# Kernel tuning notes

Measured on AMD Instinct MI355X. Metric: run time of the kernel, lower is better.

## Reference

```python
import jax, jax.numpy as jnp
import numpy as np

N, WH, C = 8, 16384, 256
R = 4
DK = 256

def setup_inputs() -> dict:
    key = jax.random.key(0)
    ks = jax.random.split(key, 11)
    s = lambda fan_in: 1.0 / np.sqrt(fan_in)
    return {
        "x":    jax.random.normal(ks[0], (N, WH, C), dtype=jnp.float32),
        # SequenceReducer linear: in=C*R, out=C (stored as [in, out])
        "w_sr": jax.random.uniform(ks[1], (C * R, C), jnp.float32, -s(C * R), s(C * R)),
        "b_sr": jax.random.uniform(ks[2], (C,), jnp.float32, -s(C * R), s(C * R)),
        # q/k/v projections: in=C, out=DK
        "w_q":  jax.random.uniform(ks[3], (C, DK), jnp.float32, -s(C), s(C)),
        "b_q":  jax.random.uniform(ks[4], (DK,), jnp.float32, -s(C), s(C)),
        "w_k":  jax.random.uniform(ks[5], (C, DK), jnp.float32, -s(C), s(C)),
        "b_k":  jax.random.uniform(ks[6], (DK,), jnp.float32, -s(C), s(C)),
        "w_v":  jax.random.uniform(ks[7], (C, DK), jnp.float32, -s(C), s(C)),
        "b_v":  jax.random.uniform(ks[8], (DK,), jnp.float32, -s(C), s(C)),
        # out projection: in=DK, out=C*R
        "w_o":  jax.random.uniform(ks[9], (DK, C * R), jnp.float32, -s(DK), s(DK)),
        "b_o":  jax.random.uniform(ks[10], (C * R,), jnp.float32, -s(DK), s(DK)),
    }

def reference(x, w_sr, b_sr, w_q, b_q, w_k, b_k, w_v, b_v, w_o, b_o):
    n, wh, c = x.shape
    L = wh // R  # reduced sequence length
    # SequenceReducer: fold R adjacent tokens into channel dim, then linear back to C
    xr = x.reshape(n, L, c * R) @ w_sr + b_sr              # [N, L, C]
    q = xr @ w_q + b_q                                     # [N, L, DK]
    k = xr @ w_k + b_k
    v = xr @ w_v + b_v
    scale = jnp.asarray(DK ** 0.5, x.dtype)
    logits = jnp.einsum('nqd,nkd->nqk', q, k) / scale      # [N, L, L]
    attn = jax.nn.softmax(logits, axis=-1)
    o = jnp.einsum('nqk,nkd->nqd', attn, v)                # [N, L, DK]
    out = (o @ w_o + b_o).reshape(n, wh, c)                # [N, WH, C]
    return out
```

## Files before the change

### kernel.cpp

```cpp
#include <hip/hip_runtime.h>

#define DEVI __device__ __forceinline__

typedef float  f32x4  __attribute__((ext_vector_type(4)));
typedef float  f32x16 __attribute__((ext_vector_type(16)));
typedef short  s16x8  __attribute__((ext_vector_type(8)));
typedef unsigned u32x4 __attribute__((ext_vector_type(4)));

DEVI void gload16(const void* g, void* l) {
  __builtin_amdgcn_global_load_lds(
      (const __attribute__((address_space(1))) void*)g,
      (__attribute__((address_space(3))) void*)l, 16, 0, 0);
}

DEVI ushort f2b(float f) {
  unsigned u = __builtin_bit_cast(unsigned, f);
  unsigned r = (u + 0x7fffu + ((u >> 16) & 1u)) >> 16;
  return (ushort)r;
}
DEVI unsigned cvtpk(float lo, float hi) {
  unsigned r;
  asm("v_cvt_pk_bf16_f32 %0, %1, %2" : "=v"(r) : "v"(lo), "v"(hi));
  return r;
}
DEVI float b2f(short s) {
  return __builtin_bit_cast(float, (unsigned)((ushort)s) << 16);
}
DEVI float max3(float a, float b, float c) { return fmaxf(fmaxf(a, b), c); }

DEVI f32x4 mfma16(s16x8 a, s16x8 b, f32x4 c) {
  return __builtin_amdgcn_mfma_f32_16x16x32_bf16(a, b, c, 0, 0, 0);
}
DEVI f32x16 mfma32(s16x8 a, s16x8 b, f32x16 c) {
  return __builtin_amdgcn_mfma_f32_32x32x16_bf16(a, b, c, 0, 0, 0);
}

DEVI int kperm(int r) {
  return (r & 0x13) | ((r & 4) << 1) | ((r & 8) >> 1);
}

__global__ __launch_bounds__(256) void k_compose(
    const float* __restrict__ w_sr, const float* __restrict__ b_sr,
    const float* __restrict__ w_q, const float* __restrict__ b_q,
    const float* __restrict__ w_k, const float* __restrict__ b_k,
    const float* __restrict__ w_v, const float* __restrict__ b_v,
    const float* __restrict__ w_o,
    ushort* __restrict__ wqkvT, ushort* __restrict__ woT, float* __restrict__ bqkv)
{
  const int b = blockIdx.x, t = threadIdx.x;
  if (b < 256) {
    const int i0 = b * 4;
    float acc[4][3] = {};
    for (int c = 0; c < 256; ++c) {
      float wq = w_q[c * 256 + t], wk = w_k[c * 256 + t], wv = w_v[c * 256 + t];
#pragma unroll
      for (int r = 0; r < 4; ++r) {
        float a = w_sr[(i0 + r) * 256 + c];
        acc[r][0] += a * wq; acc[r][1] += a * wk; acc[r][2] += a * wv;
      }
    }
#pragma unroll
    for (int r = 0; r < 4; ++r) {
      wqkvT[(size_t)(t)       * 1024 + i0 + r] = f2b(acc[r][0]);
      wqkvT[(size_t)(256 + t) * 1024 + i0 + r] = f2b(acc[r][1]);
      wqkvT[(size_t)(512 + t) * 1024 + i0 + r] = f2b(acc[r][2]);
    }
  } else if (b == 256) {
    float a0 = b_q[t], a1 = b_k[t], a2 = b_v[t];
    for (int c = 0; c < 256; ++c) {
      float bs = b_sr[c];
      a0 += bs * w_q[c * 256 + t];
      a1 += bs * w_k[c * 256 + t];
      a2 += bs * w_v[c * 256 + t];
    }
    bqkv[t] = a0; bqkv[256 + t] = a1; bqkv[512 + t] = a2;
  } else {
    const int kk = b - 257;
#pragma unroll
    for (int n = t; n < 1024; n += 256)
      woT[(size_t)n * 256 + kk] = f2b(w_o[(size_t)kk * 1024 + n]);
  }
}

__global__ __launch_bounds__(256, 2) void k_gemm_qkv(
    const float* __restrict__ X, const ushort* __restrict__ WT,
    const float* __restrict__ bias,
    ushort* __restrict__ Qo, ushort* __restrict__ Ko, ushort* __restrict__ VTo)
{
  __shared__ float  As[128 * 32];
  __shared__ ushort Bs[256 * 32];
  const int tid = threadIdx.x;
  const int l = tid & 63, w = tid >> 6;
  const int wr = w >> 1, wc = w & 1;
  const int g = l >> 4, lr = l & 15;
  const int bx = blockIdx.x;
  const int xs = (bx & 7) * 32 + (bx >> 3);
  const int tM = xs * 128, tN = blockIdx.y * 256;
  f32x4 acc[4][8] = {};

  for (int kt = 0; kt < 32; ++kt) {
    const int k0 = kt * 32;
#pragma unroll
    for (int j = 0; j < 4; ++j) {
      int chunk = j * 256 + tid;
      int row = chunk >> 3, kc = chunk & 7;
      gload16(X + (size_t)(tM + row) * 1024 + k0 + ((kc ^ (row & 7)) << 2),
              (char*)As + (j * 256 + w * 64) * 16);
    }
#pragma unroll
    for (int j = 0; j < 4; ++j) {
      int chunk = j * 256 + tid;
      int row = chunk >> 2, kc = chunk & 3;
      gload16(WT + (size_t)(tN + row) * 1024 + k0 + ((kc ^ (row & 3)) << 3),
              (char*)Bs + (j * 256 + w * 64) * 16);
    }
    __syncthreads();
    s16x8 bfr[8];
#pragma unroll
    for (int ni = 0; ni < 8; ++ni) {
      int col = wc * 128 + ni * 16 + lr;
      bfr[ni] = *(const s16x8*)&Bs[col * 32 + ((g ^ (col & 3)) << 3)];
    }
#pragma unroll
    for (int mi = 0; mi < 4; ++mi) {
      int row = wr * 64 + mi * 16 + lr;
      int c1 = (2 * g) ^ (row & 7);
      int c2 = (2 * g + 1) ^ (row & 7);
      f32x4 a0 = *(const f32x4*)&As[row * 32 + c1 * 4];
      f32x4 a1 = *(const f32x4*)&As[row * 32 + c2 * 4];
      s16x8 af = __builtin_bit_cast(s16x8,
          (u32x4){cvtpk(a0[0], a0[1]), cvtpk(a0[2], a0[3]),
                  cvtpk(a1[0], a1[1]), cvtpk(a1[2], a1[3])});
#pragma unroll
      for (int ni = 0; ni < 8; ++ni)
        acc[mi][ni] = mfma16(af, bfr[ni], acc[mi][ni]);
    }
    __syncthreads();
  }
#pragma unroll
  for (int ni = 0; ni < 8; ++ni) {
    const int col = tN + wc * 128 + ni * 16 + lr;
    const float bv = bias[col];
#pragma unroll
    for (int mi = 0; mi < 4; ++mi) {
      const int r0 = tM + wr * 64 + mi * 16 + g * 4;
      f32x4 c = acc[mi][ni];
      if (col < 512) {
        ushort* dst = (col < 256) ? Qo : Ko;
        const int cc = col & 255;
#pragma unroll
        for (int j = 0; j < 4; ++j)
          dst[(size_t)(r0 + j) * 256 + cc] = f2b(c[j] + bv);
      } else {
        const int d = col - 512;
        const int n = r0 >> 12, lrr = r0 & 4095;
        ushort4 pv;
        pv.x = f2b(c[0] + bv); pv.y = f2b(c[1] + bv);
        pv.z = f2b(c[2] + bv); pv.w = f2b(c[3] + bv);
        *(ushort4*)&VTo[(size_t)n * 256 * 4096 + (size_t)d * 4096 + lrr] = pv;
      }
    }
  }
}

#define KSC 0.0901687369f

template<int NSPLIT>
__global__ __launch_bounds__(256, 2) void k_flash(
    const ushort* __restrict__ Qg, const ushort* __restrict__ Kg,
    const ushort* __restrict__ VTg, ushort* __restrict__ Po, float* __restrict__ MLo)
{
  __shared__ ushort Ks[2][8192];
  __shared__ ushort Vs[2][8192];
  const int tid = threadIdx.x;
  const int l = tid & 63, w = tid >> 6;
  const int by = blockIdx.x & 7;
  const int rest = blockIdx.x >> 3;
  const int split = (NSPLIT == 2) ? (rest & 1) : 0;
  const int qt = (NSPLIT == 2) ? (rest >> 1) : rest;
  const int NT = (NSPLIT == 2) ? 64 : 128;
  const int kv0 = split * 2048;
  const int q0 = qt * 128 + w * 32;
  const int cl = l & 31, h = l >> 5;
  const size_t qrow = (size_t)by * 4096 + q0 + cl;

  s16x8 qf[16];
#pragma unroll
  for (int s = 0; s < 16; ++s)
    qf[s] = *(const s16x8*)&Qg[qrow * 256 + s * 16 + h * 8];

  f32x16 ot[8] = {};
  float m_run = -1e30f, l_run = 0.0f;

  const ushort* kb0 = Kg + ((size_t)by * 4096 + kv0) * 256;
  const ushort* vb0 = VTg + (size_t)by * 256 * 4096 + kv0;

  auto stage = [&](int t, int buf) {
    const ushort* kb = kb0 + t * 32 * 256;
#pragma unroll
    for (int j = 0; j < 4; ++j) {
      int chunk = j * 256 + tid;
      gload16(kb + kperm(chunk & 31) * 256 + (chunk >> 5) * 8,
              &Ks[buf][(j * 256 + w * 64) * 8]);
    }
    const ushort* vb = vb0 + t * 32;
#pragma unroll
    for (int j = 0; j < 4; ++j) {
      int chunk = j * 256 + tid;
      gload16(vb + (size_t)(chunk & 255) * 4096 + (chunk >> 8) * 8,
              &Vs[buf][(j * 256 + w * 64) * 8]);
    }
  };

  stage(0, 0);
  __syncthreads();

  for (int t = 0; t < NT; ++t) {
    const int buf = t & 1;
    if (t + 1 < NT) stage(t + 1, buf ^ 1);
    const ushort* KT = Ks[buf];

    f32x16 sa = {};
    __builtin_amdgcn_s_setprio(1);
#pragma unroll
    for (int s = 0; s < 16; ++s) {
      s16x8 a = *(const s16x8*)&KT[(2 * s + h) * 256 + cl * 8];
      sa = mfma32(a, qf[s], sa);
    }
    __builtin_amdgcn_s_setprio(0);

    float t0 = max3(sa[0], sa[1], sa[2]);
    float t1 = max3(sa[3], sa[4], sa[5]);
    float t2 = max3(sa[6], sa[7], sa[8]);
    float t3 = max3(sa[9], sa[10], sa[11]);
    float t4 = max3(sa[12], sa[13], sa[14]);
    float pmax = fmaxf(max3(t0, t1, t2), max3(t3, t4, sa[15]));
    pmax = fmaxf(pmax, __shfl_xor(pmax, 32));
    if (!__all(pmax <= m_run + 120.0f)) {
      float m_new = fmaxf(m_run, pmax);
      float corr = exp2f((m_run - m_new) * KSC);
      l_run *= corr;
#pragma unroll
      for (int mf = 0; mf < 8; ++mf)
#pragma unroll
        for (int i = 0; i < 16; ++i) ot[mf][i] *= corr;
      m_run = m_new;
    }
    const float mK = m_run * KSC;
    unsigned pk[4][2];
    float lp = 0.0f;
#pragma unroll
    for (int gq = 0; gq < 4; ++gq) {
      float p0 = exp2f(__builtin_fmaf(sa[4 * gq + 0], KSC, -mK));
      float p1 = exp2f(__builtin_fmaf(sa[4 * gq + 1], KSC, -mK));
      float p2 = exp2f(__builtin_fmaf(sa[4 * gq + 2], KSC, -mK));
      float p3 = exp2f(__builtin_fmaf(sa[4 * gq + 3], KSC, -mK));
      lp += (p0 + p1) + (p2 + p3);
      pk[gq][0] = cvtpk(p0, p1);
      pk[gq][1] = cvtpk(p2, p3);
    }
    l_run += lp;

    const ushort* VT2 = Vs[buf];
#pragma unroll
    for (int ks = 0; ks < 2; ++ks) {
      const s16x8 pf = __builtin_bit_cast(s16x8,
          (u32x4){pk[2 * ks][0], pk[2 * ks][1], pk[2 * ks + 1][0], pk[2 * ks + 1][1]});
      __builtin_amdgcn_s_setprio(1);
#pragma unroll
      for (int mf = 0; mf < 8; ++mf) {
        s16x8 va = *(const s16x8*)&VT2[(2 * ks + h) * 2048 + (mf * 32 + cl) * 8];
        ot[mf] = mfma32(va, pf, ot[mf]);
      }
      __builtin_amdgcn_s_setprio(0);
    }
    __syncthreads();
  }

  const float l_tot = l_run + __shfl_xor(l_run, 32);
  const float rl = 1.0f / l_tot;
  const size_t orow = (size_t)split * 32768 + qrow;
#pragma unroll
  for (int mf = 0; mf < 8; ++mf)
#pragma unroll
    for (int c = 0; c < 4; ++c) {
      const int d0 = mf * 32 + 8 * c + 4 * h;
      uint2 pv;
      pv.x = cvtpk(ot[mf][4 * c + 0] * rl, ot[mf][4 * c + 1] * rl);
      pv.y = cvtpk(ot[mf][4 * c + 2] * rl, ot[mf][4 * c + 3] * rl);
      *(uint2*)&Po[orow * 256 + d0] = pv;
    }
  if (NSPLIT == 2 && h == 0) {
    float2 ml; ml.x = m_run; ml.y = l_tot;
    *(float2*)&MLo[orow * 2] = ml;
  }
}

__global__ __launch_bounds__(256) void k_combine(
    const ushort* __restrict__ P, const float* __restrict__ ML,
    ushort* __restrict__ Og)
{
  const int idx = blockIdx.x * 256 + threadIdx.x;
  const int r = idx >> 5, dc = (idx & 31) * 8;
  const float m0 = ML[(size_t)r * 2],             l0 = ML[(size_t)r * 2 + 1];
  const float m1 = ML[(size_t)(32768 + r) * 2],   l1 = ML[(size_t)(32768 + r) * 2 + 1];
  const float m  = fmaxf(m0, m1);
  const float a0 = l0 * exp2f((m0 - m) * KSC);
  const float a1 = l1 * exp2f((m1 - m) * KSC);
  const float inv = 1.0f / (a0 + a1);
  const float w0 = a0 * inv, w1 = a1 * inv;
  s16x8 x0 = *(const s16x8*)&P[(size_t)r * 256 + dc];
  s16x8 x1 = *(const s16x8*)&P[(size_t)(32768 + r) * 256 + dc];
  union { ushort u[8]; s16x8 v; } o;
#pragma unroll
  for (int j = 0; j < 8; ++j)
    o.u[j] = f2b(w0 * b2f(x0[j]) + w1 * b2f(x1[j]));
  *(s16x8*)&Og[(size_t)r * 256 + dc] = o.v;
}

__global__ __launch_bounds__(256, 2) void k_gemm_out(
    const ushort* __restrict__ Oi, const ushort* __restrict__ WT,
    const float* __restrict__ bias, float* __restrict__ OUT)
{
  __shared__ ushort As[128 * 32];
  __shared__ ushort Bs[256 * 32];
  const int tid = threadIdx.x;
  const int l = tid & 63, w = tid >> 6;
  const int wr = w >> 1, wc = w & 1;
  const int g = l >> 4, lr = l & 15;
  const int tM = blockIdx.x * 128, tN = blockIdx.y * 256;
  f32x4 acc[4][8] = {};

  for (int kt = 0; kt < 8; ++kt) {
    const int k0 = kt * 32;
#pragma unroll
    for (int j = 0; j < 2; ++j) {
      int chunk = j * 256 + tid;
      int row = chunk >> 2, kc = chunk & 3;
      gload16(Oi + (size_t)(tM + row) * 256 + k0 + ((kc ^ (row & 3)) << 3),
              (char*)As + (j * 256 + w * 64) * 16);
    }
#pragma unroll
    for (int j = 0; j < 4; ++j) {
      int chunk = j * 256 + tid;
      int row = chunk >> 2, kc = chunk & 3;
      gload16(WT + (size_t)(tN + row) * 256 + k0 + ((kc ^ (row & 3)) << 3),
              (char*)Bs + (j * 256 + w * 64) * 16);
    }
    __syncthreads();
    s16x8 afr[4], bfr[8];
#pragma unroll
    for (int ni = 0; ni < 8; ++ni) {
      int col = wc * 128 + ni * 16 + lr;
      bfr[ni] = *(const s16x8*)&Bs[col * 32 + ((g ^ (col & 3)) << 3)];
    }
#pragma unroll
    for (int mi = 0; mi < 4; ++mi) {
      int row = wr * 64 + mi * 16 + lr;
      afr[mi] = *(const s16x8*)&As[row * 32 + ((g ^ (row & 3)) << 3)];
    }
#pragma unroll
    for (int mi = 0; mi < 4; ++mi)
#pragma unroll
      for (int ni = 0; ni < 8; ++ni)
        acc[mi][ni] = mfma16(afr[mi], bfr[ni], acc[mi][ni]);
    __syncthreads();
  }
#pragma unroll
  for (int ni = 0; ni < 8; ++ni) {
    const int col = tN + wc * 128 + ni * 16 + lr;
    const float bv = bias[col];
#pragma unroll
    for (int mi = 0; mi < 4; ++mi) {
      const int r0 = tM + wr * 64 + mi * 16 + g * 4;
      f32x4 c = acc[mi][ni];
#pragma unroll
      for (int j = 0; j < 4; ++j)
        OUT[(size_t)(r0 + j) * 1024 + col] = c[j] + bv;
    }
  }
}

extern "C" void kernel_launch(void* const* d_in, const int* in_sizes, int n_in,
                              void* d_out, int out_size, void* d_ws, size_t ws_size,
                              hipStream_t stream) {
  const float* x    = (const float*)d_in[0];
  const float* w_sr = (const float*)d_in[1];
  const float* b_sr = (const float*)d_in[2];
  const float* w_q  = (const float*)d_in[3];
  const float* b_q  = (const float*)d_in[4];
  const float* w_k  = (const float*)d_in[5];
  const float* b_k  = (const float*)d_in[6];
  const float* w_v  = (const float*)d_in[7];
  const float* b_v  = (const float*)d_in[8];
  const float* w_o  = (const float*)d_in[9];
  const float* b_o  = (const float*)d_in[10];
  float* out = (float*)d_out;

  char* ws = (char*)d_ws;
  const size_t MB = 1024 * 1024;
  const bool split = ws_size >= 84 * MB;

  ushort* Q  = (ushort*)(ws);
  ushort* K  = (ushort*)(ws + 16 * MB);
  ushort* VT = (ushort*)(ws + 32 * MB);
  ushort* P  = (ushort*)(ws + 48 * MB);
  float*  ML = (float*) (ws + 80 * MB);
  ushort* WQKVT = split ? (ushort*)(ws + 80 * MB + 512 * 1024) : (ushort*)(ws + 64 * MB);
  ushort* WOT   = split ? (ushort*)(ws + 82 * MB + 512 * 1024) : (ushort*)(ws + 66 * MB);
  float*  BQKV  = split ? (float*) (ws + 83 * MB)              : (float*) (ws + 66 * MB + 512 * 1024);

  k_compose<<<513, 256, 0, stream>>>(w_sr, b_sr, w_q, b_q, w_k, b_k, w_v, b_v,
                                     w_o, WQKVT, WOT, BQKV);
  k_gemm_qkv<<<dim3(256, 3), 256, 0, stream>>>(x, WQKVT, BQKV, Q, K, VT);
  if (split) {
    k_flash<2><<<512, 256, 0, stream>>>(Q, K, VT, P, ML);
    k_combine<<<4096, 256, 0, stream>>>(P, ML, P);
  } else {
    k_flash<1><<<256, 256, 0, stream>>>(Q, K, VT, P, nullptr);
  }
  k_gemm_out<<<dim3(256, 4), 256, 0, stream>>>(P, WOT, b_o, out);
}
```

Baseline: 355.0 us.

## Split fused SR+QKV GEMM into separate reducer and QKV projection GEMMs

Before, the sequence reducer weight was folded into the Q/K/V weights, so one GEMM with K=1024 ran over all 768 output columns. Now the reducer GEMM (K=1024, 256 outputs) writes an intermediate bf16 XR, and a second GEMM (K=256, 768 outputs) produces Q/K/V from it. This cuts total MACs roughly in half and replaces the per-block weight-compose kernel with a plain transpose/convert prep. The cost is an extra bf16 round-trip of XR through memory and one more kernel launch, plus an extra bf16 rounding step that may change numerics.

```diff
diff --git a/kernel.cpp b/kernel.cpp
--- a/kernel.cpp
+++ b/kernel.cpp
@@ -39,55 +39,109 @@
   return (r & 0x13) | ((r & 4) << 1) | ((r & 8) >> 1);
 }
 
-__global__ __launch_bounds__(256) void k_compose(
-    const float* __restrict__ w_sr, const float* __restrict__ b_sr,
+__global__ __launch_bounds__(256) void k_prep(
+    const float* __restrict__ w_sr,
     const float* __restrict__ w_q, const float* __restrict__ b_q,
     const float* __restrict__ w_k, const float* __restrict__ b_k,
     const float* __restrict__ w_v, const float* __restrict__ b_v,
     const float* __restrict__ w_o,
-    ushort* __restrict__ wqkvT, ushort* __restrict__ woT, float* __restrict__ bqkv)
+    ushort* __restrict__ wsrT, ushort* __restrict__ wqkvT,
+    ushort* __restrict__ woT, float* __restrict__ bqkv)
 {
   const int b = blockIdx.x, t = threadIdx.x;
-  if (b < 256) {
-    const int i0 = b * 4;
-    float acc[4][3] = {};
-    for (int c = 0; c < 256; ++c) {
-      float wq = w_q[c * 256 + t], wk = w_k[c * 256 + t], wv = w_v[c * 256 + t];
-#pragma unroll
-      for (int r = 0; r < 4; ++r) {
-        float a = w_sr[(i0 + r) * 256 + c];
-        acc[r][0] += a * wq; acc[r][1] += a * wk; acc[r][2] += a * wv;
-      }
-    }
-#pragma unroll
-    for (int r = 0; r < 4; ++r) {
-      wqkvT[(size_t)(t)       * 1024 + i0 + r] = f2b(acc[r][0]);
-      wqkvT[(size_t)(256 + t) * 1024 + i0 + r] = f2b(acc[r][1]);
-      wqkvT[(size_t)(512 + t) * 1024 + i0 + r] = f2b(acc[r][2]);
-    }
-  } else if (b == 256) {
-    float a0 = b_q[t], a1 = b_k[t], a2 = b_v[t];
-    for (int c = 0; c < 256; ++c) {
-      float bs = b_sr[c];
-      a0 += bs * w_q[c * 256 + t];
-      a1 += bs * w_k[c * 256 + t];
-      a2 += bs * w_v[c * 256 + t];
-    }
-    bqkv[t] = a0; bqkv[256 + t] = a1; bqkv[512 + t] = a2;
+  if (b < 1024) {
+    int o = b * 256 + t;
+    int n = o >> 10, k = o & 1023;
+    wsrT[o] = f2b(w_sr[k * 256 + n]);
+  } else if (b < 1792) {
+    int o = (b - 1024) * 256 + t;
+    int n = o >> 8, k = o & 255;
+    const float* w = (n < 256) ? w_q : (n < 512) ? w_k : w_v;
+    wqkvT[o] = f2b(w[k * 256 + (n & 255)]);
+  } else if (b < 2816) {
+    int o = (b - 1792) * 256 + t;
+    int n = o >> 8, k = o & 255;
+    woT[o] = f2b(w_o[k * 1024 + n]);
   } else {
-    const int kk = b - 257;
-#pragma unroll
-    for (int n = t; n < 1024; n += 256)
-      woT[(size_t)n * 256 + kk] = f2b(w_o[(size_t)kk * 1024 + n]);
-  }
-}
-
-__global__ __launch_bounds__(256, 2) void k_gemm_qkv(
+    bqkv[t] = b_q[t]; bqkv[256 + t] = b_k[t]; bqkv[512 + t] = b_v[t];
+  }
+}
+
+__global__ __launch_bounds__(256, 2) void k_gemm_sr(
     const float* __restrict__ X, const ushort* __restrict__ WT,
+    const float* __restrict__ bias, ushort* __restrict__ XR)
+{
+  __shared__ float  As[128 * 32];
+  __shared__ ushort Bs[256 * 32];
+  const int tid = threadIdx.x;
+  const int l = tid & 63, w = tid >> 6;
+  const int wr = w >> 1, wc = w & 1;
+  const int g = l >> 4, lr = l & 15;
+  const int bx = blockIdx.x;
+  const int xs = (bx & 7) * 32 + (bx >> 3);
+  const int tM = xs * 128;
+  f32x4 acc[4][8] = {};
+
+  for (int kt = 0; kt < 32; ++kt) {
+    const int k0 = kt * 32;
+#pragma unroll
+    for (int j = 0; j < 4; ++j) {
+      int chunk = j * 256 + tid;
+      int row = chunk >> 3, kc = chunk & 7;
+      gload16(X + (size_t)(tM + row) * 1024 + k0 + ((kc ^ (row & 7)) << 2),
+              (char*)As + (j * 256 + w * 64) * 16);
+    }
+#pragma unroll
+    for (int j = 0; j < 4; ++j) {
+      int chunk = j * 256 + tid;
+      int row = chunk >> 2, kc = chunk & 3;
+      gload16(WT + (size_t)row * 1024 + k0 + ((kc ^ (row & 3)) << 3),
+              (char*)Bs + (j * 256 + w * 64) * 16);
+    }
+    __syncthreads();
+    s16x8 bfr[8];
+#pragma unroll
+    for (int ni = 0; ni < 8; ++ni) {
+      int col = wc * 128 + ni * 16 + lr;
+      bfr[ni] = *(const s16x8*)&Bs[col * 32 + ((g ^ (col & 3)) << 3)];
+    }
+#pragma unroll
+    for (int mi = 0; mi < 4; ++mi) {
+      int row = wr * 64 + mi * 16 + lr;
+      int c1 = (2 * g) ^ (row & 7);
+      int c2 = (2 * g + 1) ^ (row & 7);
+      f32x4 a0 = *(const f32x4*)&As[row * 32 + c1 * 4];
+      f32x4 a1 = *(const f32x4*)&As[row * 32 + c2 * 4];
+      s16x8 af = __builtin_bit_cast(s16x8,
+          (u32x4){cvtpk(a0[0], a0[1]), cvtpk(a0[2], a0[3]),
+                  cvtpk(a1[0], a1[1]), cvtpk(a1[2], a1[3])});
+#pragma unroll
+      for (int ni = 0; ni < 8; ++ni)
+        acc[mi][ni] = mfma16(af, bfr[ni], acc[mi][ni]);
+    }
+    __syncthreads();
+  }
+#pragma unroll
+  for (int ni = 0; ni < 8; ++ni) {
+    const int col = wc * 128 + ni * 16 + lr;
+    const float bv = bias[col];
+#pragma unroll
+    for (int mi = 0; mi < 4; ++mi) {
+      const int r0 = tM + wr * 64 + mi * 16 + g * 4;
+      f32x4 c = acc[mi][ni];
+#pragma unroll
+      for (int j = 0; j < 4; ++j)
+        XR[(size_t)(r0 + j) * 256 + col] = f2b(c[j] + bv);
+    }
+  }
+}
+
+__global__ __launch_bounds__(256, 2) void k_gemm_qkv2(
+    const ushort* __restrict__ XR, const ushort* __restrict__ WT,
     const float* __restrict__ bias,
     ushort* __restrict__ Qo, ushort* __restrict__ Ko, ushort* __restrict__ VTo)
 {
-  __shared__ float  As[128 * 32];
+  __shared__ ushort As[128 * 32];
   __shared__ ushort Bs[256 * 32];
   const int tid = threadIdx.x;
   const int l = tid & 63, w = tid >> 6;
@@ -98,24 +152,24 @@
   const int tM = xs * 128, tN = blockIdx.y * 256;
   f32x4 acc[4][8] = {};
 
-  for (int kt = 0; kt < 32; ++kt) {
+  for (int kt = 0; kt < 8; ++kt) {
     const int k0 = kt * 32;
 #pragma unroll
-    for (int j = 0; j < 4; ++j) {
-      int chunk = j * 256 + tid;
-      int row = chunk >> 3, kc = chunk & 7;
-      gload16(X + (size_t)(tM + row) * 1024 + k0 + ((kc ^ (row & 7)) << 2),
+    for (int j = 0; j < 2; ++j) {
+      int chunk = j * 256 + tid;
+      int row = chunk >> 2, kc = chunk & 3;
+      gload16(XR + (size_t)(tM + row) * 256 + k0 + ((kc ^ (row & 3)) << 3),
               (char*)As + (j * 256 + w * 64) * 16);
     }
 #pragma unroll
     for (int j = 0; j < 4; ++j) {
       int chunk = j * 256 + tid;
       int row = chunk >> 2, kc = chunk & 3;
-      gload16(WT + (size_t)(tN + row) * 1024 + k0 + ((kc ^ (row & 3)) << 3),
+      gload16(WT + (size_t)(tN + row) * 256 + k0 + ((kc ^ (row & 3)) << 3),
               (char*)Bs + (j * 256 + w * 64) * 16);
     }
     __syncthreads();
-    s16x8 bfr[8];
+    s16x8 afr[4], bfr[8];
 #pragma unroll
     for (int ni = 0; ni < 8; ++ni) {
       int col = wc * 128 + ni * 16 + lr;
@@ -124,40 +178,35 @@
 #pragma unroll
     for (int mi = 0; mi < 4; ++mi) {
       int row = wr * 64 + mi * 16 + lr;
-      int c1 = (2 * g) ^ (row & 7);
-      int c2 = (2 * g + 1) ^ (row & 7);
-      f32x4 a0 = *(const f32x4*)&As[row * 32 + c1 * 4];
-      f32x4 a1 = *(const f32x4*)&As[row * 32 + c2 * 4];
-      s16x8 af = __builtin_bit_cast(s16x8,
-          (u32x4){cvtpk(a0[0], a0[1]), cvtpk(a0[2], a0[3]),
-                  cvtpk(a1[0], a1[1]), cvtpk(a1[2], a1[3])});
+      afr[mi] = *(const s16x8*)&As[row * 32 + ((g ^ (row & 3)) << 3)];
+    }
+#pragma unroll
+    for (int mi = 0; mi < 4; ++mi)
 #pragma unroll
       for (int ni = 0; ni < 8; ++ni)
-        acc[mi][ni] = mfma16(af, bfr[ni], acc[mi][ni]);
-    }
-    __syncthreads();
-  }
+        acc[mi][ni] = mfma16(afr[mi], bfr[ni], acc[mi][ni]);
+    __syncthreads();
+  }
+  const int strip = blockIdx.y;
 #pragma unroll
   for (int ni = 0; ni < 8; ++ni) {
-    const int col = tN + wc * 128 + ni * 16 + lr;
-    const float bv = bias[col];
+    const int cc = wc * 128 + ni * 16 + lr;
+    const float bv = bias[tN + cc];
 #pragma unroll
     for (int mi = 0; mi < 4; ++mi) {
       const int r0 = tM + wr * 64 + mi * 16 + g * 4;
       f32x4 c = acc[mi][ni];
-      if (col < 512) {
-        ushort* dst = (col < 256) ? Qo : Ko;
-        const int cc = col & 255;
+      if (strip < 2) {
+        ushort* dst = strip ? Ko : Qo;
 #pragma unroll
         for (int j = 0; j < 4; ++j)
           dst[(size_t)(r0 + j) * 256 + cc] = f2b(c[j] + bv);
       } else {
-        const int d = col - 512;
         const int n = r0 >> 12, lrr = r0 & 4095;
         ushort4 pv;
         pv.x = f2b(c[0] + bv); pv.y = f2b(c[1] + bv);
         pv.z = f2b(c[2] + bv); pv.w = f2b(c[3] + bv);
-        *(ushort4*)&VTo[(size_t)n * 256 * 4096 + (size_t)d * 4096 + lrr] = pv;
+        *(ushort4*)&VTo[(size_t)n * 256 * 4096 + (size_t)cc * 4096 + lrr] = pv;
       }
     }
   }
@@ -399,20 +448,25 @@
 
   char* ws = (char*)d_ws;
   const size_t MB = 1024 * 1024;
+  const size_t KB = 1024;
   const bool split = ws_size >= 84 * MB;
 
   ushort* Q  = (ushort*)(ws);
   ushort* K  = (ushort*)(ws + 16 * MB);
   ushort* VT = (ushort*)(ws + 32 * MB);
+  ushort* XR = (ushort*)(ws + 48 * MB);
   ushort* P  = (ushort*)(ws + 48 * MB);
-  float*  ML = (float*) (ws + 80 * MB);
-  ushort* WQKVT = split ? (ushort*)(ws + 80 * MB + 512 * 1024) : (ushort*)(ws + 64 * MB);
-  ushort* WOT   = split ? (ushort*)(ws + 82 * MB + 512 * 1024) : (ushort*)(ws + 66 * MB);
-  float*  BQKV  = split ? (float*) (ws + 83 * MB)              : (float*) (ws + 66 * MB + 512 * 1024);
-
-  k_compose<<<513, 256, 0, stream>>>(w_sr, b_sr, w_q, b_q, w_k, b_k, w_v, b_v,
-                                     w_o, WQKVT, WOT, BQKV);
-  k_gemm_qkv<<<dim3(256, 3), 256, 0, stream>>>(x, WQKVT, BQKV, Q, K, VT);
+  float*  ML    = (float*) (ws + 80 * MB);
+  char*   wbase = split ? (ws + 80 * MB + 512 * KB) : (ws + 64 * MB);
+  ushort* WSRT  = (ushort*)(wbase);
+  ushort* WQKVT = (ushort*)(wbase + 512 * KB);
+  ushort* WOT   = (ushort*)(wbase + 1024 * KB);
+  float*  BQKV  = (float*) (wbase + 1536 * KB);
+
+  k_prep<<<2817, 256, 0, stream>>>(w_sr, w_q, b_q, w_k, b_k, w_v, b_v, w_o,
+                                   WSRT, WQKVT, WOT, BQKV);
+  k_gemm_sr<<<256, 256, 0, stream>>>(x, WSRT, b_sr, XR);
+  k_gemm_qkv2<<<dim3(256, 3), 256, 0, stream>>>(XR, WQKVT, BQKV, Q, K, VT);
   if (split) {
     k_flash<2><<<512, 256, 0, stream>>>(Q, K, VT, P, ML);
     k_combine<<<4096, 256, 0, stream>>>(P, ML, P);
```

After: 321.6 us. 1.1x faster.
